# Kernel tuning notes

Hardware: AMD Instinct MI355X
Metric: run time of the kernel (lower is better)

The kernel has to match this reference:

```python
import jax, jax.numpy as jnp
import numpy as np

N, E, F_IN, H, L = 1536, 49152, 27, 64, 32


def _ln(x, g, b, eps=1e-5):
    m = x.mean(-1, keepdims=True)
    v = ((x - m) ** 2).mean(-1, keepdims=True)
    return (x - m) * jax.lax.rsqrt(v + eps) * g + b


def _gatv2(x, src, dst, Wl, bl, Wr, br, att, bias, n):
    # PyG GATv2Conv, heads=1: alpha_ij = softmax_j( att . leaky_relu(Wl x_j + Wr x_i) )
    xl = x @ Wl + bl  # source transform [n,H]
    xr = x @ Wr + br  # target transform [n,H]
    e = jax.nn.leaky_relu(xl[src] + xr[dst], 0.2)  # [E',H]
    s = e @ att  # [E'] attention logits
    m = jax.ops.segment_max(s, dst, num_segments=n)
    w = jnp.exp(s - m[dst])
    denom = jax.ops.segment_sum(w, dst, num_segments=n)
    alpha = w / denom[dst]
    return jax.ops.segment_sum(alpha[:, None] * xl[src], dst, num_segments=n) + bias


def _model(x, eps_nodes, eps_graph, edge_index,
           Wl1, bl1, Wr1, br1, att1, bias1,
           Wl2, bl2, Wr2, br2, att2, bias2,
           Wnm, bnm, Wnv, bnv, Wgm, bgm, Wgv, bgv,
           Wd1, bd1, ln1_g, ln1_b, Wd2, bd2, ln2_g, ln2_b, Wd3, bd3,
           We1, be1, lne_g, lne_b, We2, be2,
           Wf1, bf1, lnf_g, lnf_b, Wf2, bf2):
    n = x.shape[0]
    loop = jnp.arange(n)
    src = jnp.concatenate([edge_index[0], loop])  # add self loops (PyG default)
    dst = jnp.concatenate([edge_index[1], loop])
    h = jax.nn.relu(_gatv2(x, src, dst, Wl1, bl1, Wr1, br1, att1, bias1, n))
    h = jax.nn.relu(_gatv2(h, src, dst, Wl2, bl2, Wr2, br2, att2, bias2, n))
    node_mu = h @ Wnm + bnm
    node_logvar = h @ Wnv + bnv
    gh = h.mean(0)
    graph_mu = gh @ Wgm + bgm
    graph_logvar = gh @ Wgv + bgv
    z = node_mu + eps_nodes * jnp.exp(0.5 * node_logvar)  # node reparam (training)
    _zg = graph_mu + eps_graph * jnp.exp(0.5 * graph_logvar)  # z_graph: computed, unused downstream as in source
    # dec_node_features MLP
    nf = _ln(jax.nn.relu(z @ Wd1 + bd1), ln1_g, ln1_b)
    nf = _ln(jax.nn.relu(nf @ Wd2 + bd2), ln2_g, ln2_b)
    nf = nf @ Wd3 + bd3  # [n, F_IN]
    # feature_refinement (node_embeddings = h is passed in forward)
    nf = _ln(jax.nn.relu(jnp.concatenate([nf, h], -1) @ Wf1 + bf1), lnf_g, lnf_b)
    node_features = nf @ Wf2 + bf2
    # edge_pred over all i<j pairs, vectorized (replaces the O(N^2) python loop)
    iu, ju = jnp.triu_indices(n, k=1)
    ei = jnp.concatenate([z[iu], z[ju]], -1)  # [P, 2L]
    eh = _ln(jax.nn.relu(ei @ We1 + be1), lne_g, lne_b)
    edge_logits = (eh @ We2 + be2)[:, 0]  # [P]
    return node_features, edge_logits, node_mu, node_logvar, graph_mu, graph_logvar


def setup_inputs() -> dict:
    key = jax.random.key(0)
    ki = iter(jax.random.split(key, 40))
    def W(fi, fo):
        return jax.random.normal(next(ki), (fi, fo), jnp.float32) / np.sqrt(fi)
    z64 = jnp.zeros((H,), jnp.float32)
    o64 = jnp.ones((H,), jnp.float32)
    zL = jnp.zeros((L,), jnp.float32)
    zF = jnp.zeros((F_IN,), jnp.float32)
    inp = {}
    inp["x"] = jax.random.normal(next(ki), (N, F_IN), jnp.float32)
    inp["edge_index"] = jax.random.randint(next(ki), (2, E), 0, N)
    inp["eps_nodes"] = jax.random.normal(next(ki), (N, L), jnp.float32)
    inp["eps_graph"] = jax.random.normal(next(ki), (L,), jnp.float32)
    inp.update(Wl1=W(F_IN, H), bl1=z64, Wr1=W(F_IN, H), br1=z64,
               att1=jax.random.normal(next(ki), (H,), jnp.float32) / np.sqrt(H), bias1=z64,
               Wl2=W(H, H), bl2=z64, Wr2=W(H, H), br2=z64,
               att2=jax.random.normal(next(ki), (H,), jnp.float32) / np.sqrt(H), bias2=z64)
    inp.update(Wnm=W(H, L), bnm=zL, Wnv=W(H, L), bnv=zL,
               Wgm=W(H, L), bgm=zL, Wgv=W(H, L), bgv=zL)
    inp.update(Wd1=W(L, H), bd1=z64, ln1_g=o64, ln1_b=z64,
               Wd2=W(H, H), bd2=z64, ln2_g=o64, ln2_b=z64,
               Wd3=W(H, F_IN), bd3=zF)
    inp.update(We1=W(2 * L, H), be1=z64, lne_g=o64, lne_b=z64,
               We2=W(H, 1), be2=jnp.zeros((1,), jnp.float32))
    inp.update(Wf1=W(F_IN + H, H), bf1=z64, lnf_g=o64, lnf_b=z64,
               Wf2=W(H, F_IN), bf2=zF)
    return inp


def reference(x, edge_index, eps_nodes, eps_graph,
              Wl1, bl1, Wr1, br1, att1, bias1,
              Wl2, bl2, Wr2, br2, att2, bias2,
              Wnm, bnm, Wnv, bnv, Wgm, bgm, Wgv, bgv,
              Wd1, bd1, ln1_g, ln1_b, Wd2, bd2, ln2_g, ln2_b, Wd3, bd3,
              We1, be1, lne_g, lne_b, We2, be2,
              Wf1, bf1, lnf_g, lnf_b, Wf2, bf2):
    return _model(x, eps_nodes, eps_graph, edge_index,
                  Wl1, bl1, Wr1, br1, att1, bias1,
                  Wl2, bl2, Wr2, br2, att2, bias2,
                  Wnm, bnm, Wnv, bnv, Wgm, bgm, Wgv, bgv,
                  Wd1, bd1, ln1_g, ln1_b, Wd2, bd2, ln2_g, ln2_b, Wd3, bd3,
                  We1, be1, lne_g, lne_b, We2, be2,
                  Wf1, bf1, lnf_g, lnf_b, Wf2, bf2)
```

## Files before the change

kernel.cpp:

```cpp
#include <hip/hip_runtime.h>

#define NN 1536
#define NE 49152
#define NM (NE + NN)
#define FIN 27
#define HD 64
#define LDIM 32
#define PP 1178880

#define EL_OFF  (NN*FIN)
#define MU_OFF  (EL_OFF + PP)
#define LV_OFF  (MU_OFF + NN*LDIM)
#define GMU_OFF (LV_OFF + NN*LDIM)
#define GLV_OFF (GMU_OFF + LDIM)

__device__ __forceinline__ float wsum(float v) {
#pragma unroll
  for (int m = 1; m < 64; m <<= 1) v += __shfl_xor(v, m, 64);
  return v;
}
__device__ __forceinline__ void wsum2(float& a, float& b) {
#pragma unroll
  for (int m = 1; m < 64; m <<= 1) {
    a += __shfl_xor(a, m, 64);
    b += __shfl_xor(b, m, 64);
  }
}
__device__ __forceinline__ float lnorm64(float x, float g, float b) {
  float s1 = x, s2 = x * x;
  wsum2(s1, s2);
  float mu = s1 * (1.0f / 64.0f);
  float var = fmaf(-mu, mu, s2 * (1.0f / 64.0f));
  return (x - mu) * rsqrtf(var + 1e-5f) * g + b;
}
__device__ __forceinline__ void cp4(float* dst, const float* __restrict__ src,
                                    int n4, int t) {
  const float4* s4 = (const float4*)src;
  float4* d4 = (float4*)dst;
  for (int e = t; e < n4; e += 256) d4[e] = s4[e];
}

template <int KIN, bool FUSE>
__global__ __launch_bounds__(256) void gvae_xform(
    const float* __restrict__ in, const float* __restrict__ Dn,
    const float* __restrict__ hbias,
    const float* __restrict__ Wl, const float* __restrict__ bl,
    const float* __restrict__ Wr, const float* __restrict__ br,
    float* __restrict__ xl, float* __restrict__ xr) {
  __shared__ __align__(16) float sWl[KIN * HD];
  __shared__ __align__(16) float sWr[KIN * HD];
  int t = threadIdx.x;
  cp4(sWl, Wl, KIN * 16, t);
  cp4(sWr, Wr, KIN * 16, t);
  int i = blockIdx.x * 4 + (t >> 6);
  int k = t & 63;
  float xv = (k < KIN) ? in[i * KIN + k] : 0.f;
  if (FUSE) xv = fmaxf(xv / Dn[i] + hbias[k], 0.f);
  float l0 = bl[k], l1 = 0.f, r0 = br[k], r1 = 0.f;
  __syncthreads();
#pragma unroll
  for (int a = 0; a < KIN; a += 2) {
    float xa = __shfl(xv, a, 64);
    l0 = fmaf(xa, sWl[a * HD + k], l0);
    r0 = fmaf(xa, sWr[a * HD + k], r0);
    if (a + 1 < KIN) {
      float xb = __shfl(xv, a + 1, 64);
      l1 = fmaf(xb, sWl[(a + 1) * HD + k], l1);
      r1 = fmaf(xb, sWr[(a + 1) * HD + k], r1);
    }
  }
  xl[i * HD + k] = l0 + l1;
  xr[i * HD + k] = r0 + r1;
}

__global__ __launch_bounds__(256) void gvae_edgepass(
    const int* __restrict__ ei,
    const float* __restrict__ xl, const float* __restrict__ xr,
    const float* __restrict__ att,
    float* __restrict__ A, float* __restrict__ D) {
  int m = blockIdx.x * 4 + (threadIdx.x >> 6);
  int lane = threadIdx.x & 63;
  int src, dst;
  if (m < NE) { src = ei[m]; dst = ei[NE + m]; }
  else        { src = m - NE; dst = m - NE; }
  float xls = xl[src * HD + lane];
  float e = xls + xr[dst * HD + lane];
  e = fmaxf(e, 0.2f * e);
  float w = expf(wsum(e * att[lane]));
  atomicAdd(&A[dst * HD + lane], w * xls);
  if (lane == 0) atomicAdd(&D[dst], w);
}

#define oNM 0
#define oNV 2048
#define oE1 4096
#define oD1 8192
#define oD2 10240
#define oD3 14336
#define oF1 16064
#define oF2 21888
#define SWTOT 23616

__global__ __launch_bounds__(256) void gvae_node(
    const float* __restrict__ A2, const float* __restrict__ D2,
    const float* __restrict__ bias2,
    const float* __restrict__ eps,
    const float* __restrict__ Wnm, const float* __restrict__ bnm,
    const float* __restrict__ Wnv, const float* __restrict__ bnv,
    const float* __restrict__ We1, const float* __restrict__ be1,
    const float* __restrict__ Wd1, const float* __restrict__ bd1,
    const float* __restrict__ g1, const float* __restrict__ b1,
    const float* __restrict__ Wd2, const float* __restrict__ bd2,
    const float* __restrict__ g2, const float* __restrict__ b2,
    const float* __restrict__ Wd3, const float* __restrict__ bd3,
    const float* __restrict__ Wf1, const float* __restrict__ bf1,
    const float* __restrict__ gf, const float* __restrict__ bfv,
    const float* __restrict__ Wf2, const float* __restrict__ bf2,
    float* __restrict__ uo, float* __restrict__ vo,
    float* __restrict__ gh, float* __restrict__ out) {
  __shared__ __align__(16) float sW[SWTOT];
  __shared__ float ghred[256];
  int t = threadIdx.x;
  cp4(sW + oNM, Wnm, 512, t);
  cp4(sW + oNV, Wnv, 512, t);
  cp4(sW + oE1, We1, 1024, t);
  cp4(sW + oD1, Wd1, 512, t);
  cp4(sW + oD2, Wd2, 1024, t);
  cp4(sW + oD3, Wd3, 432, t);
  cp4(sW + oF1, Wf1, 1456, t);
  cp4(sW + oF2, Wf2, 432, t);

  int i = blockIdx.x * 4 + (t >> 6);
  int k = t & 63;
  int kk = k & 31;
  int kc = (k < FIN) ? k : (FIN - 1);
  float h2k = fmaxf(A2[i * HD + k] / D2[i] + bias2[k], 0.f);
  ghred[t] = h2k;
  __syncthreads();
  if (t < 64) {
    float s = (ghred[t] + ghred[t + 64]) + (ghred[t + 128] + ghred[t + 192]);
    atomicAdd(&gh[t], s * (1.0f / NN));
  }

  const float* W = sW + ((k < 32) ? oNM : oNV);
  float c0 = (k < 32) ? bnm[kk] : bnv[kk];
  float c1 = 0.f, c2 = 0.f, c3 = 0.f;
#pragma unroll
  for (int a = 0; a < HD; a += 4) {
    c0 = fmaf(__shfl(h2k, a, 64),     W[a * LDIM + kk],       c0);
    c1 = fmaf(__shfl(h2k, a + 1, 64), W[(a + 1) * LDIM + kk], c1);
    c2 = fmaf(__shfl(h2k, a + 2, 64), W[(a + 2) * LDIM + kk], c2);
    c3 = fmaf(__shfl(h2k, a + 3, 64), W[(a + 3) * LDIM + kk], c3);
  }
  float acc = (c0 + c1) + (c2 + c3);
  if (k < 32) out[MU_OFF + i * LDIM + kk] = acc;
  else        out[LV_OFF + i * LDIM + kk] = acc;

  float lv = __shfl(acc, k + 32, 64);
  float zk = acc + eps[i * LDIM + kk] * expf(0.5f * lv);

  float u0 = be1[k], u1 = 0.f, v0 = 0.f, v1 = 0.f;
#pragma unroll
  for (int a = 0; a < LDIM; a += 2) {
    float za = __shfl(zk, a, 64);
    float zb = __shfl(zk, a + 1, 64);
    u0 = fmaf(za, sW[oE1 + a * HD + k], u0);
    u1 = fmaf(zb, sW[oE1 + (a + 1) * HD + k], u1);
    v0 = fmaf(za, sW[oE1 + (a + LDIM) * HD + k], v0);
    v1 = fmaf(zb, sW[oE1 + (a + 1 + LDIM) * HD + k], v1);
  }
  uo[i * HD + k] = u0 + u1;
  vo[i * HD + k] = v0 + v1;

  c0 = bd1[k]; c1 = 0.f; c2 = 0.f; c3 = 0.f;
#pragma unroll
  for (int a = 0; a < LDIM; a += 4) {
    c0 = fmaf(__shfl(zk, a, 64),     sW[oD1 + a * HD + k],       c0);
    c1 = fmaf(__shfl(zk, a + 1, 64), sW[oD1 + (a + 1) * HD + k], c1);
    c2 = fmaf(__shfl(zk, a + 2, 64), sW[oD1 + (a + 2) * HD + k], c2);
    c3 = fmaf(__shfl(zk, a + 3, 64), sW[oD1 + (a + 3) * HD + k], c3);
  }
  float nf1 = lnorm64(fmaxf((c0 + c1) + (c2 + c3), 0.f), g1[k], b1[k]);

  c0 = bd2[k]; c1 = 0.f; c2 = 0.f; c3 = 0.f;
#pragma unroll
  for (int a = 0; a < HD; a += 4) {
    c0 = fmaf(__shfl(nf1, a, 64),     sW[oD2 + a * HD + k],       c0);
    c1 = fmaf(__shfl(nf1, a + 1, 64), sW[oD2 + (a + 1) * HD + k], c1);
    c2 = fmaf(__shfl(nf1, a + 2, 64), sW[oD2 + (a + 2) * HD + k], c2);
    c3 = fmaf(__shfl(nf1, a + 3, 64), sW[oD2 + (a + 3) * HD + k], c3);
  }
  float nf2 = lnorm64(fmaxf((c0 + c1) + (c2 + c3), 0.f), g2[k], b2[k]);

  c0 = 0.f; c1 = 0.f; c2 = 0.f; c3 = 0.f;
#pragma unroll
  for (int a = 0; a < HD; a += 4) {
    c0 = fmaf(__shfl(nf2, a, 64),     sW[oD3 + a * FIN + kc],       c0);
    c1 = fmaf(__shfl(nf2, a + 1, 64), sW[oD3 + (a + 1) * FIN + kc], c1);
    c2 = fmaf(__shfl(nf2, a + 2, 64), sW[oD3 + (a + 2) * FIN + kc], c2);
    c3 = fmaf(__shfl(nf2, a + 3, 64), sW[oD3 + (a + 3) * FIN + kc], c3);
  }
  float nf3 = (k < FIN) ? ((c0 + c1) + (c2 + c3) + bd3[kc]) : 0.f;

  c0 = bf1[k]; c1 = 0.f; c2 = 0.f; c3 = 0.f;
#pragma unroll
  for (int j = 0; j < FIN; j++) {
    float nj = __shfl(nf3, j, 64);
    c0 = fmaf(nj, sW[oF1 + j * HD + k], c0);
  }
#pragma unroll
  for (int a = 0; a < HD; a += 4) {
    c0 = fmaf(__shfl(h2k, a, 64),     sW[oF1 + (FIN + a) * HD + k],     c0);
    c1 = fmaf(__shfl(h2k, a + 1, 64), sW[oF1 + (FIN + a + 1) * HD + k], c1);
    c2 = fmaf(__shfl(h2k, a + 2, 64), sW[oF1 + (FIN + a + 2) * HD + k], c2);
    c3 = fmaf(__shfl(h2k, a + 3, 64), sW[oF1 + (FIN + a + 3) * HD + k], c3);
  }
  float rr = lnorm64(fmaxf((c0 + c1) + (c2 + c3), 0.f), gf[k], bfv[k]);

  c0 = 0.f; c1 = 0.f; c2 = 0.f; c3 = 0.f;
#pragma unroll
  for (int a = 0; a < HD; a += 4) {
    c0 = fmaf(__shfl(rr, a, 64),     sW[oF2 + a * FIN + kc],       c0);
    c1 = fmaf(__shfl(rr, a + 1, 64), sW[oF2 + (a + 1) * FIN + kc], c1);
    c2 = fmaf(__shfl(rr, a + 2, 64), sW[oF2 + (a + 2) * FIN + kc], c2);
    c3 = fmaf(__shfl(rr, a + 3, 64), sW[oF2 + (a + 3) * FIN + kc], c3);
  }
  if (k < FIN) out[i * FIN + k] = (c0 + c1) + (c2 + c3) + bf2[kc];
}

__global__ void gvae_ghead(const float* __restrict__ gh,
                           const float* __restrict__ Wgm, const float* __restrict__ bgm,
                           const float* __restrict__ Wgv, const float* __restrict__ bgv,
                           float* __restrict__ out) {
  int k = threadIdx.x;
  int kk = k & 31;
  float ghk = gh[k];
  const float* W = (k < 32) ? Wgm : Wgv;
  float c0 = (k < 32) ? bgm[kk] : bgv[kk];
  float c1 = 0.f, c2 = 0.f, c3 = 0.f;
#pragma unroll
  for (int a = 0; a < HD; a += 4) {
    c0 = fmaf(__shfl(ghk, a, 64),     W[a * LDIM + kk],       c0);
    c1 = fmaf(__shfl(ghk, a + 1, 64), W[(a + 1) * LDIM + kk], c1);
    c2 = fmaf(__shfl(ghk, a + 2, 64), W[(a + 2) * LDIM + kk], c2);
    c3 = fmaf(__shfl(ghk, a + 3, 64), W[(a + 3) * LDIM + kk], c3);
  }
  float acc = (c0 + c1) + (c2 + c3);
  if (k < 32) out[GMU_OFF + kk] = acc;
  else        out[GLV_OFF + kk] = acc;
}

__global__ __launch_bounds__(256) void gvae_edge(
    const float* __restrict__ u, const float* __restrict__ v,
    const float* __restrict__ lng, const float* __restrict__ lnb,
    const float* __restrict__ w2, const float* __restrict__ be2,
    float* __restrict__ out) {
  int bj = blockIdx.x, bi = blockIdx.y;
  if (bi > bj) return;
  __shared__ float U[64 * 64];
  __shared__ float V[64 * 68];
  __shared__ float C[64];
  __shared__ float cc[2];
  int t = threadIdx.x;
  const float4* u4p = (const float4*)(u + bi * 64 * HD);
  const float4* v4p = (const float4*)(v + bj * 64 * HD);
#pragma unroll
  for (int it = 0; it < 4; ++it) {
    int r = t + it * 256;
    int row = r >> 4, q = r & 15;
    float4 uu = u4p[r];
    *(float4*)&U[row * 64 + q * 4] = uu;
    float4 vv = v4p[r];
    *(float4*)&V[row * 68 + q * 4] = vv;
  }
  if (t < 64) {
    float ck = lng[t] * w2[t];
    C[t] = ck;
    float cb = lnb[t] * w2[t];
    float sC = wsum(ck);
    float sB = wsum(cb);
    if (t == 0) { cc[0] = sC; cc[1] = sB + be2[0]; }
  }
  __syncthreads();
  float C1 = cc[0], C0 = cc[1];

  int w = t >> 6, lane = t & 63;
  float S1[16], S2[16], Sc[16];
#pragma unroll
  for (int ii = 0; ii < 16; ii++) { S1[ii] = 0.f; S2[ii] = 0.f; Sc[ii] = 0.f; }
  const float* Ub = &U[(w * 16) * 64];
  for (int k4 = 0; k4 < 16; k4++) {
    float4 v4 = *(const float4*)&V[lane * 68 + k4 * 4];
    float4 c4 = *(const float4*)&C[k4 * 4];
#pragma unroll
    for (int ii = 0; ii < 16; ii++) {
      float4 u4 = *(const float4*)&Ub[ii * 64 + k4 * 4];
      float t0 = fmaxf(u4.x + v4.x, 0.f);
      float t1 = fmaxf(u4.y + v4.y, 0.f);
      float t2 = fmaxf(u4.z + v4.z, 0.f);
      float t3 = fmaxf(u4.w + v4.w, 0.f);
      S1[ii] += (t0 + t1) + (t2 + t3);
      S2[ii] = fmaf(t0, t0, fmaf(t1, t1, fmaf(t2, t2, fmaf(t3, t3, S2[ii]))));
      Sc[ii] = fmaf(t0, c4.x, fmaf(t1, c4.y, fmaf(t2, c4.z, fmaf(t3, c4.w, Sc[ii]))));
    }
  }
  int j = bj * 64 + lane;
  const float inv64 = 1.0f / 64.0f;
#pragma unroll
  for (int ii = 0; ii < 16; ii++) {
    int i = bi * 64 + w * 16 + ii;
    if (j > i) {
      int pbase = i * (2 * NN - i - 1) / 2 - i - 1;
      float mu = S1[ii] * inv64;
      float var = fmaf(-mu, mu, S2[ii] * inv64);
      float logit = (Sc[ii] - mu * C1) * rsqrtf(var + 1e-5f) + C0;
      out[pbase + j] = logit;
    }
  }
}

extern "C" void kernel_launch(void* const* d_in, const int* in_sizes, int n_in,
                              void* d_out, int out_size, void* d_ws, size_t ws_size,
                              hipStream_t stream) {
  const float* x    = (const float*)d_in[0];
  const int*   ei   = (const int*)d_in[1];
  const float* eps  = (const float*)d_in[2];
  const float* Wl1  = (const float*)d_in[4];
  const float* bl1  = (const float*)d_in[5];
  const float* Wr1  = (const float*)d_in[6];
  const float* br1  = (const float*)d_in[7];
  const float* att1 = (const float*)d_in[8];
  const float* bias1= (const float*)d_in[9];
  const float* Wl2  = (const float*)d_in[10];
  const float* bl2  = (const float*)d_in[11];
  const float* Wr2  = (const float*)d_in[12];
  const float* br2  = (const float*)d_in[13];
  const float* att2 = (const float*)d_in[14];
  const float* bias2= (const float*)d_in[15];
  const float* Wnm  = (const float*)d_in[16];
  const float* bnm  = (const float*)d_in[17];
  const float* Wnv  = (const float*)d_in[18];
  const float* bnv  = (const float*)d_in[19];
  const float* Wgm  = (const float*)d_in[20];
  const float* bgm  = (const float*)d_in[21];
  const float* Wgv  = (const float*)d_in[22];
  const float* bgv  = (const float*)d_in[23];
  const float* Wd1  = (const float*)d_in[24];
  const float* bd1  = (const float*)d_in[25];
  const float* ln1g = (const float*)d_in[26];
  const float* ln1b = (const float*)d_in[27];
  const float* Wd2  = (const float*)d_in[28];
  const float* bd2  = (const float*)d_in[29];
  const float* ln2g = (const float*)d_in[30];
  const float* ln2b = (const float*)d_in[31];
  const float* Wd3  = (const float*)d_in[32];
  const float* bd3  = (const float*)d_in[33];
  const float* We1  = (const float*)d_in[34];
  const float* be1  = (const float*)d_in[35];
  const float* lneg = (const float*)d_in[36];
  const float* lneb = (const float*)d_in[37];
  const float* We2  = (const float*)d_in[38];
  const float* be2  = (const float*)d_in[39];
  const float* Wf1  = (const float*)d_in[40];
  const float* bf1  = (const float*)d_in[41];
  const float* lnfg = (const float*)d_in[42];
  const float* lnfb = (const float*)d_in[43];
  const float* Wf2  = (const float*)d_in[44];
  const float* bf2  = (const float*)d_in[45];
  float* out = (float*)d_out;

  float* fb  = (float*)d_ws;
  float* xl1 = fb;
  float* xr1 = xl1 + NN * HD;
  float* xl2 = xr1 + NN * HD;
  float* xr2 = xl2 + NN * HD;
  float* uu  = xr2 + NN * HD;
  float* vv  = uu  + NN * HD;
  float* A1  = vv  + NN * HD;
  float* A2  = A1  + NN * HD;
  float* D1  = A2  + NN * HD;
  float* D2  = D1  + NN;
  float* gh  = D2  + NN;
  size_t zbytes = (size_t)(2 * NN * HD + 2 * NN + HD) * sizeof(float);

  hipMemsetAsync(A1, 0, zbytes, stream);

  gvae_xform<FIN, false><<<NN / 4, 256, 0, stream>>>(x, nullptr, nullptr,
                                                     Wl1, bl1, Wr1, br1, xl1, xr1);
  gvae_edgepass<<<NM / 4, 256, 0, stream>>>(ei, xl1, xr1, att1, A1, D1);
  gvae_xform<HD, true><<<NN / 4, 256, 0, stream>>>(A1, D1, bias1,
                                                   Wl2, bl2, Wr2, br2, xl2, xr2);
  gvae_edgepass<<<NM / 4, 256, 0, stream>>>(ei, xl2, xr2, att2, A2, D2);

  gvae_node<<<NN / 4, 256, 0, stream>>>(A2, D2, bias2, eps,
      Wnm, bnm, Wnv, bnv, We1, be1,
      Wd1, bd1, ln1g, ln1b, Wd2, bd2, ln2g, ln2b, Wd3, bd3,
      Wf1, bf1, lnfg, lnfb, Wf2, bf2,
      uu, vv, gh, out);
  gvae_ghead<<<1, 64, 0, stream>>>(gh, Wgm, bgm, Wgv, bgv, out);
  gvae_edge<<<dim3(24, 24), 256, 0, stream>>>(uu, vv, lneg, lneb, We2, be2, out + EL_OFF);
}
```

Before: 259.7 us.

## Fold memset and graph head into kernels, compact edge grid, trim node smem

```diff
diff --git a/kernel.cpp b/kernel.cpp
--- a/kernel.cpp
+++ b/kernel.cpp
@@ -40,16 +40,22 @@
   for (int e = t; e < n4; e += 256) d4[e] = s4[e];
 }
 
-template <int KIN, bool FUSE>
+template <int KIN, bool FUSE, bool ZERO>
 __global__ __launch_bounds__(256) void gvae_xform(
     const float* __restrict__ in, const float* __restrict__ Dn,
     const float* __restrict__ hbias,
     const float* __restrict__ Wl, const float* __restrict__ bl,
     const float* __restrict__ Wr, const float* __restrict__ br,
-    float* __restrict__ xl, float* __restrict__ xr) {
+    float* __restrict__ xl, float* __restrict__ xr,
+    float* __restrict__ zbase, int nz4) {
   __shared__ __align__(16) float sWl[KIN * HD];
   __shared__ __align__(16) float sWr[KIN * HD];
   int t = threadIdx.x;
+  if (ZERO) {
+    float4 zz = {0.f, 0.f, 0.f, 0.f};
+    float4* z4 = (float4*)zbase;
+    for (int e = blockIdx.x * 256 + t; e < nz4; e += (NN / 4) * 256) z4[e] = zz;
+  }
   cp4(sWl, Wl, KIN * 16, t);
   cp4(sWr, Wr, KIN * 16, t);
   int i = blockIdx.x * 4 + (t >> 6);
@@ -82,7 +88,7 @@
   int lane = threadIdx.x & 63;
   int src, dst;
   if (m < NE) { src = ei[m]; dst = ei[NE + m]; }
-  else        { src = m - NE; dst = m - NE; }
+  else        { src = m - NE; dst = src; }
   float xls = xl[src * HD + lane];
   float e = xls + xr[dst * HD + lane];
   e = fmaxf(e, 0.2f * e);
@@ -91,17 +97,13 @@
   if (lane == 0) atomicAdd(&D[dst], w);
 }
 
-#define oNM 0
-#define oNV 2048
-#define oE1 4096
-#define oD1 8192
-#define oD2 10240
-#define oD3 14336
-#define oF1 16064
-#define oF2 21888
-#define SWTOT 23616
-
-__global__ __launch_bounds__(256) void gvae_node(
+#define oE1 0
+#define oD1 4096
+#define oD2 6144
+#define oF1 10240
+#define SWTOT 16064
+
+__global__ __launch_bounds__(256, 2) void gvae_node(
     const float* __restrict__ A2, const float* __restrict__ D2,
     const float* __restrict__ bias2,
     const float* __restrict__ eps,
@@ -121,14 +123,10 @@
   __shared__ __align__(16) float sW[SWTOT];
   __shared__ float ghred[256];
   int t = threadIdx.x;
-  cp4(sW + oNM, Wnm, 512, t);
-  cp4(sW + oNV, Wnv, 512, t);
   cp4(sW + oE1, We1, 1024, t);
   cp4(sW + oD1, Wd1, 512, t);
   cp4(sW + oD2, Wd2, 1024, t);
-  cp4(sW + oD3, Wd3, 432, t);
   cp4(sW + oF1, Wf1, 1456, t);
-  cp4(sW + oF2, Wf2, 432, t);
 
   int i = blockIdx.x * 4 + (t >> 6);
   int k = t & 63;
@@ -142,7 +140,7 @@
     atomicAdd(&gh[t], s * (1.0f / NN));
   }
 
-  const float* W = sW + ((k < 32) ? oNM : oNV);
+  const float* W = (k < 32) ? Wnm : Wnv;
   float c0 = (k < 32) ? bnm[kk] : bnv[kk];
   float c1 = 0.f, c2 = 0.f, c3 = 0.f;
 #pragma unroll
@@ -195,10 +193,10 @@
   c0 = 0.f; c1 = 0.f; c2 = 0.f; c3 = 0.f;
 #pragma unroll
   for (int a = 0; a < HD; a += 4) {
-    c0 = fmaf(__shfl(nf2, a, 64),     sW[oD3 + a * FIN + kc],       c0);
-    c1 = fmaf(__shfl(nf2, a + 1, 64), sW[oD3 + (a + 1) * FIN + kc], c1);
-    c2 = fmaf(__shfl(nf2, a + 2, 64), sW[oD3 + (a + 2) * FIN + kc], c2);
-    c3 = fmaf(__shfl(nf2, a + 3, 64), sW[oD3 + (a + 3) * FIN + kc], c3);
+    c0 = fmaf(__shfl(nf2, a, 64),     Wd3[a * FIN + kc],       c0);
+    c1 = fmaf(__shfl(nf2, a + 1, 64), Wd3[(a + 1) * FIN + kc], c1);
+    c2 = fmaf(__shfl(nf2, a + 2, 64), Wd3[(a + 2) * FIN + kc], c2);
+    c3 = fmaf(__shfl(nf2, a + 3, 64), Wd3[(a + 3) * FIN + kc], c3);
   }
   float nf3 = (k < FIN) ? ((c0 + c1) + (c2 + c3) + bd3[kc]) : 0.f;
 
@@ -220,48 +218,51 @@
   c0 = 0.f; c1 = 0.f; c2 = 0.f; c3 = 0.f;
 #pragma unroll
   for (int a = 0; a < HD; a += 4) {
-    c0 = fmaf(__shfl(rr, a, 64),     sW[oF2 + a * FIN + kc],       c0);
-    c1 = fmaf(__shfl(rr, a + 1, 64), sW[oF2 + (a + 1) * FIN + kc], c1);
-    c2 = fmaf(__shfl(rr, a + 2, 64), sW[oF2 + (a + 2) * FIN + kc], c2);
-    c3 = fmaf(__shfl(rr, a + 3, 64), sW[oF2 + (a + 3) * FIN + kc], c3);
+    c0 = fmaf(__shfl(rr, a, 64),     Wf2[a * FIN + kc],       c0);
+    c1 = fmaf(__shfl(rr, a + 1, 64), Wf2[(a + 1) * FIN + kc], c1);
+    c2 = fmaf(__shfl(rr, a + 2, 64), Wf2[(a + 2) * FIN + kc], c2);
+    c3 = fmaf(__shfl(rr, a + 3, 64), Wf2[(a + 3) * FIN + kc], c3);
   }
   if (k < FIN) out[i * FIN + k] = (c0 + c1) + (c2 + c3) + bf2[kc];
-}
-
-__global__ void gvae_ghead(const float* __restrict__ gh,
-                           const float* __restrict__ Wgm, const float* __restrict__ bgm,
-                           const float* __restrict__ Wgv, const float* __restrict__ bgv,
-                           float* __restrict__ out) {
-  int k = threadIdx.x;
-  int kk = k & 31;
-  float ghk = gh[k];
-  const float* W = (k < 32) ? Wgm : Wgv;
-  float c0 = (k < 32) ? bgm[kk] : bgv[kk];
-  float c1 = 0.f, c2 = 0.f, c3 = 0.f;
-#pragma unroll
-  for (int a = 0; a < HD; a += 4) {
-    c0 = fmaf(__shfl(ghk, a, 64),     W[a * LDIM + kk],       c0);
-    c1 = fmaf(__shfl(ghk, a + 1, 64), W[(a + 1) * LDIM + kk], c1);
-    c2 = fmaf(__shfl(ghk, a + 2, 64), W[(a + 2) * LDIM + kk], c2);
-    c3 = fmaf(__shfl(ghk, a + 3, 64), W[(a + 3) * LDIM + kk], c3);
-  }
-  float acc = (c0 + c1) + (c2 + c3);
-  if (k < 32) out[GMU_OFF + kk] = acc;
-  else        out[GLV_OFF + kk] = acc;
 }
 
 __global__ __launch_bounds__(256) void gvae_edge(
     const float* __restrict__ u, const float* __restrict__ v,
     const float* __restrict__ lng, const float* __restrict__ lnb,
     const float* __restrict__ w2, const float* __restrict__ be2,
+    const float* __restrict__ gh,
+    const float* __restrict__ Wgm, const float* __restrict__ bgm,
+    const float* __restrict__ Wgv, const float* __restrict__ bgv,
     float* __restrict__ out) {
-  int bj = blockIdx.x, bi = blockIdx.y;
-  if (bi > bj) return;
   __shared__ float U[64 * 64];
   __shared__ float V[64 * 68];
   __shared__ float C[64];
   __shared__ float cc[2];
   int t = threadIdx.x;
+  int wv = t >> 6, lane = t & 63;
+
+  if (blockIdx.x == 0 && wv == 3) {
+    int kk = lane & 31;
+    float ghk = gh[lane];
+    const float* W = (lane < 32) ? Wgm : Wgv;
+    float c0 = (lane < 32) ? bgm[kk] : bgv[kk];
+    float c1 = 0.f, c2 = 0.f, c3 = 0.f;
+#pragma unroll
+    for (int a = 0; a < HD; a += 4) {
+      c0 = fmaf(__shfl(ghk, a, 64),     W[a * LDIM + kk],       c0);
+      c1 = fmaf(__shfl(ghk, a + 1, 64), W[(a + 1) * LDIM + kk], c1);
+      c2 = fmaf(__shfl(ghk, a + 2, 64), W[(a + 2) * LDIM + kk], c2);
+      c3 = fmaf(__shfl(ghk, a + 3, 64), W[(a + 3) * LDIM + kk], c3);
+    }
+    float acc = (c0 + c1) + (c2 + c3);
+    if (lane < 32) out[GMU_OFF + kk] = acc;
+    else           out[GLV_OFF + kk] = acc;
+  }
+
+  int rem = blockIdx.x, bi = 0;
+  while (rem >= 24 - bi) { rem -= 24 - bi; bi++; }
+  int bj = bi + rem;
+
   const float4* u4p = (const float4*)(u + bi * 64 * HD);
   const float4* v4p = (const float4*)(v + bj * 64 * HD);
 #pragma unroll
@@ -284,11 +285,10 @@
   __syncthreads();
   float C1 = cc[0], C0 = cc[1];
 
-  int w = t >> 6, lane = t & 63;
   float S1[16], S2[16], Sc[16];
 #pragma unroll
   for (int ii = 0; ii < 16; ii++) { S1[ii] = 0.f; S2[ii] = 0.f; Sc[ii] = 0.f; }
-  const float* Ub = &U[(w * 16) * 64];
+  const float* Ub = &U[(wv * 16) * 64];
   for (int k4 = 0; k4 < 16; k4++) {
     float4 v4 = *(const float4*)&V[lane * 68 + k4 * 4];
     float4 c4 = *(const float4*)&C[k4 * 4];
@@ -308,13 +308,13 @@
   const float inv64 = 1.0f / 64.0f;
 #pragma unroll
   for (int ii = 0; ii < 16; ii++) {
-    int i = bi * 64 + w * 16 + ii;
+    int i = bi * 64 + wv * 16 + ii;
     if (j > i) {
       int pbase = i * (2 * NN - i - 1) / 2 - i - 1;
       float mu = S1[ii] * inv64;
       float var = fmaf(-mu, mu, S2[ii] * inv64);
       float logit = (Sc[ii] - mu * C1) * rsqrtf(var + 1e-5f) + C0;
-      out[pbase + j] = logit;
+      out[EL_OFF + pbase + j] = logit;
     }
   }
 }
@@ -381,15 +381,13 @@
   float* D1  = A2  + NN * HD;
   float* D2  = D1  + NN;
   float* gh  = D2  + NN;
-  size_t zbytes = (size_t)(2 * NN * HD + 2 * NN + HD) * sizeof(float);
-
-  hipMemsetAsync(A1, 0, zbytes, stream);
-
-  gvae_xform<FIN, false><<<NN / 4, 256, 0, stream>>>(x, nullptr, nullptr,
-                                                     Wl1, bl1, Wr1, br1, xl1, xr1);
+  int nz4 = (2 * NN * HD + 2 * NN + HD) / 4;
+
+  gvae_xform<FIN, false, true><<<NN / 4, 256, 0, stream>>>(
+      x, nullptr, nullptr, Wl1, bl1, Wr1, br1, xl1, xr1, A1, nz4);
   gvae_edgepass<<<NM / 4, 256, 0, stream>>>(ei, xl1, xr1, att1, A1, D1);
-  gvae_xform<HD, true><<<NN / 4, 256, 0, stream>>>(A1, D1, bias1,
-                                                   Wl2, bl2, Wr2, br2, xl2, xr2);
+  gvae_xform<HD, true, false><<<NN / 4, 256, 0, stream>>>(
+      A1, D1, bias1, Wl2, bl2, Wr2, br2, xl2, xr2, nullptr, 0);
   gvae_edgepass<<<NM / 4, 256, 0, stream>>>(ei, xl2, xr2, att2, A2, D2);
 
   gvae_node<<<NN / 4, 256, 0, stream>>>(A2, D2, bias2, eps,
@@ -397,6 +395,6 @@
       Wd1, bd1, ln1g, ln1b, Wd2, bd2, ln2g, ln2b, Wd3, bd3,
       Wf1, bf1, lnfg, lnfb, Wf2, bf2,
       uu, vv, gh, out);
-  gvae_ghead<<<1, 64, 0, stream>>>(gh, Wgm, bgm, Wgv, bgv, out);
-  gvae_edge<<<dim3(24, 24), 256, 0, stream>>>(uu, vv, lneg, lneb, We2, be2, out + EL_OFF);
-}
+  gvae_edge<<<300, 256, 0, stream>>>(uu, vv, lneg, lneb, We2, be2,
+                                     gh, Wgm, bgm, Wgv, bgv, out);
+}
```

After: 256.2 us. No clear change (-1.4%).
